# Kernel optimization log

Measured on AMD Instinct MI355X. Metric: run time of the kernel, lower is better.

Reference implementation:

```python
import jax, jax.numpy as jnp
import numpy as np
from functools import partial

VOCAB, D, H, L, T_MAX = 32000, 1024, 16, 8, 1024
HD = D // H
HIDDEN = int(D * 2.67)  # 2734, matches int(n_embd*hidden_mult)


def setup_inputs() -> dict:
    key = jax.random.key(0)
    ks = jax.random.split(key, 9)
    s = 0.02
    return {
        "idx": jax.random.randint(ks[0], (2, 1024), 0, VOCAB),
        "W_emb": jax.random.normal(ks[1], (VOCAB, D), jnp.float32) * s,  # tied with lm_head
        "norm1_w": jnp.ones((L, D), jnp.float32),
        "Wqkv": jax.random.normal(ks[2], (L, D, 3 * D), jnp.float32) * s,
        "Wout": jax.random.normal(ks[3], (L, D, D), jnp.float32) * s,
        "norm2_w": jnp.ones((L, D), jnp.float32),
        "Wg": jax.random.normal(ks[4], (L, D, HIDDEN), jnp.float32) * s,
        "Wu": jax.random.normal(ks[5], (L, D, HIDDEN), jnp.float32) * s,
        "Wd": jax.random.normal(ks[6], (L, HIDDEN, D), jnp.float32) * s,
        "final_norm_w": jnp.ones((D,), jnp.float32),
    }


def _rmsnorm(x, w, eps=1e-6):
    rms = jnp.sqrt(jnp.mean(x * x, axis=-1, keepdims=True) + eps)
    return x / rms * w


def _rope(x, cos_f, sin_f):
    # x: [B,H,T,hd]; cos_f/sin_f: [T, hd//2]
    x1, x2 = x[..., : HD // 2], x[..., HD // 2 :]
    c = cos_f[None, None]
    s = sin_f[None, None]
    return jnp.concatenate([x1 * c - x2 * s, x1 * s + x2 * c], axis=-1)


def _forward(idx, W_emb, norm1_w, Wqkv, Wout, norm2_w, Wg, Wu, Wd, final_norm_w):
    B, T = idx.shape
    # RoPE tables (buffers in the torch module)
    inv_freq = 1.0 / (10000.0 ** (jnp.arange(0, HD, 2, dtype=jnp.float32) / HD))
    ang = jnp.arange(T, dtype=jnp.float32)[:, None] * inv_freq[None, :]  # [T, hd//2]
    cos_f, sin_f = jnp.cos(ang), jnp.sin(ang)
    causal = jnp.tril(jnp.ones((T, T), dtype=bool))  # [T,T]
    scale = 1.0 / jnp.sqrt(jnp.float32(HD))

    def block(x, params):
        n1, wqkv, wout, n2, wg, wu, wd = params
        h = _rmsnorm(x, n1)
        qkv = (h @ wqkv).reshape(B, T, 3, H, HD).transpose(2, 0, 3, 1, 4)  # [3,B,H,T,hd]
        q, k, v = qkv[0], qkv[1], qkv[2]
        q = _rope(q, cos_f, sin_f)
        k = _rope(k, cos_f, sin_f)
        attn = jnp.einsum("bhqd,bhkd->bhqk", q, k) * scale
        attn = jnp.where(causal[None, None], attn, -jnp.inf)
        attn = jax.nn.softmax(attn, axis=-1)
        o = jnp.einsum("bhqk,bhkd->bhqd", attn, v)
        o = o.transpose(0, 2, 1, 3).reshape(B, T, D) @ wout
        x = x + o
        h2 = _rmsnorm(x, n2)
        x = x + (jax.nn.silu(h2 @ wg) * (h2 @ wu)) @ wd
        return x, None

    x = W_emb[idx]  # [B,T,D]
    x, _ = jax.lax.scan(block, x, (norm1_w, Wqkv, Wout, norm2_w, Wg, Wu, Wd))
    x = _rmsnorm(x, final_norm_w)
    return x @ W_emb.T  # tied lm_head -> [B,T,VOCAB]


def reference(idx, W_emb, norm1_w, Wqkv, Wout, norm2_w, Wg, Wu, Wd, final_norm_w):
    return _forward(idx, W_emb, norm1_w, Wqkv, Wout, norm2_w, Wg, Wu, Wd, final_norm_w)
```

## Files before the change

kernel.cpp:

```cpp
#include <hip/hip_runtime.h>
#include <cstdint>
#include <cmath>

#define D_MODEL 1024
#define T_SEQ   1024
#define NHEAD   16
#define NLAYER  8
#define HID     2734
#define HID_PAD 2816
#define NTOK    2048
#define VOCAB   32000

typedef __bf16 bf16x8 __attribute__((ext_vector_type(8)));
typedef __bf16 bf16x4 __attribute__((ext_vector_type(4)));
typedef float  f32x4  __attribute__((ext_vector_type(4)));

__device__ inline bf16x4 to_bf4(float a, float b, float c, float d) {
  bf16x4 t; t[0] = (__bf16)a; t[1] = (__bf16)b; t[2] = (__bf16)c; t[3] = (__bf16)d; return t;
}

__device__ inline void gload16(const __bf16* g, __bf16* l) {
  __builtin_amdgcn_global_load_lds(
      (const __attribute__((address_space(1))) void*)g,
      (__attribute__((address_space(3))) void*)l, 16, 0, 0);
}

__global__ __launch_bounds__(256) void embed_kernel(const int* __restrict__ idx,
                                                    const float* __restrict__ W,
                                                    float* __restrict__ x) {
  int t = blockIdx.x;
  int v = idx[t];
  float4 val = *(const float4*)&W[(size_t)v * D_MODEL + threadIdx.x * 4];
  *(float4*)&x[(size_t)t * D_MODEL + threadIdx.x * 4] = val;
}

__global__ __launch_bounds__(256) void rmsnorm_kernel(const float* __restrict__ x,
                                                      const float* __restrict__ w,
                                                      __bf16* __restrict__ out) {
  int row = blockIdx.x;
  int tid = threadIdx.x;
  float4 v = *(const float4*)&x[(size_t)row * D_MODEL + tid * 4];
  float s = v.x * v.x + v.y * v.y + v.z * v.z + v.w * v.w;
#pragma unroll
  for (int m = 32; m >= 1; m >>= 1) s += __shfl_xor(s, m, 64);
  __shared__ float red[4];
  if ((tid & 63) == 0) red[tid >> 6] = s;
  __syncthreads();
  float tot = red[0] + red[1] + red[2] + red[3];
  float inv = rsqrtf(tot * (1.0f / (float)D_MODEL) + 1e-6f);
  float4 wv = *(const float4*)&w[tid * 4];
  bf16x4 o4 = to_bf4(v.x * inv * wv.x, v.y * inv * wv.y, v.z * inv * wv.z, v.w * inv * wv.w);
  *(bf16x4*)&out[(size_t)row * D_MODEL + tid * 4] = o4;
}

__global__ __launch_bounds__(256) void rope_table_kernel(float* __restrict__ tab) {
  int p = blockIdx.x * 256 + threadIdx.x;
  int t = p >> 5, i = p & 31;
  float freq = exp2f(-(float)i * (13.287712379549449f / 32.0f));
  float sn, cs;
  sincosf((float)t * freq, &sn, &cs);
  tab[p] = cs;
  tab[32768 + p] = sn;
}

__global__ __launch_bounds__(256) void transpose_bf16_kernel(
    const float* __restrict__ in, __bf16* __restrict__ out,
    int R, int C, int Ro, int rmul, int roff) {
  __shared__ __bf16 tile[64][65];
  int r0 = blockIdx.x * 64, c0 = blockIdx.y * 64;
  int tid = threadIdx.x;
  bool fullc = (c0 + 64 <= C);
#pragma unroll
  for (int i = 0; i < 4; ++i) {
    int ri = i * 16 + (tid >> 4);
    int ci = (tid & 15) * 4;
    int r = r0 + ri;
    float4 v = {0.f, 0.f, 0.f, 0.f};
    if (r < R) {
      const float* p = in + (size_t)r * C + c0 + ci;
      if (fullc) {
        v = *(const float4*)p;
      } else {
        int c = c0 + ci;
        if (c + 0 < C) v.x = p[0];
        if (c + 1 < C) v.y = p[1];
        if (c + 2 < C) v.z = p[2];
        if (c + 3 < C) v.w = p[3];
      }
    }
    tile[ri][ci + 0] = (__bf16)v.x;
    tile[ri][ci + 1] = (__bf16)v.y;
    tile[ri][ci + 2] = (__bf16)v.z;
    tile[ri][ci + 3] = (__bf16)v.w;
  }
  __syncthreads();
#pragma unroll
  for (int i = 0; i < 4; ++i) {
    int oc = i * 16 + (tid >> 4);
    int orr = (tid & 15) * 4;
    bf16x4 t;
    t[0] = tile[orr + 0][oc];
    t[1] = tile[orr + 1][oc];
    t[2] = tile[orr + 2][oc];
    t[3] = tile[orr + 3][oc];
    *(bf16x4*)&out[((size_t)(c0 + oc) * rmul + roff) * Ro + r0 + orr] = t;
  }
}

__global__ __launch_bounds__(256) void convert_bf16_kernel(const float* __restrict__ in,
                                                           __bf16* __restrict__ out, int n4) {
  for (int i = blockIdx.x * 256 + threadIdx.x; i < n4; i += gridDim.x * 256) {
    float4 v = ((const float4*)in)[i];
    ((bf16x4*)out)[i] = to_bf4(v.x, v.y, v.z, v.w);
  }
}

template <int BM, int BN, int WM, int WN, int EPI>
__global__ __launch_bounds__(WM * WN * 64, 2) void gemm8(
    const __bf16* __restrict__ A, const __bf16* __restrict__ B,
    const float* __restrict__ Cin, void* __restrict__ Cout,
    int K, int ldc) {
  constexpr int NTH = WM * WN * 64;
  constexpr int MF = BM / (16 * WM);
  constexpr int MG = (MF + 3) / 4;
  constexpr int LA = (BM * 4) / NTH;
  constexpr int LB = (BN * 4) / NTH;
  static_assert(BN / WN == 64, "NF must be 4");
  __shared__ __align__(16) __bf16 lds[(BM + BN) * 128];

  const int tid = threadIdx.x;
  const int lane = tid & 63, wid = tid >> 6;
  const int wr = wid / WN, wn = wid % WN;
  const int lr = lane & 15, lg = lane >> 4;

  const int gx = gridDim.x;
  const int nwg = gx * gridDim.y;
  const int orig = blockIdx.y * gx + blockIdx.x;
  const int q = nwg >> 3, r8 = nwg & 7;
  const int xcd = orig & 7, loc = orig >> 3;
  const int swz = ((xcd < r8) ? xcd * (q + 1) : r8 * (q + 1) + (xcd - r8) * q) + loc;
  const int brow = (swz % gx) * BM;
  const int bcol = (swz / gx) * BN;

  const __bf16* pAg[LA];
  const __bf16* pBg[LB];
  int opA[LA], opB[LB];
#pragma unroll
  for (int i = 0; i < LA; ++i) {
    int p = tid + i * NTH;
    int row = ((p >> 6) << 4) | (p & 15), j = (p >> 4) & 3;
    pAg[i] = A + (size_t)(brow + row) * K + j * 8;
    opA[i] = p * 8;
  }
#pragma unroll
  for (int i = 0; i < LB; ++i) {
    int p = tid + i * NTH;
    int row = ((p >> 6) << 4) | (p & 15), j = (p >> 4) & 3;
    pBg[i] = B + (size_t)(bcol + row) * K + j * 8;
    opB[i] = p * 8;
  }

  const int ntiles = K >> 6;

  auto STAGE = [&](int v, int kkq) {
    int vs = v < ntiles ? v : ntiles - 1;
    int ko = vs * 64 + kkq * 32;
    int sa = (v & 1) * (BM * 64) + kkq * (BM * 32);
    int sb = BM * 128 + (v & 1) * (BN * 64) + kkq * (BN * 32);
#pragma unroll
    for (int i = 0; i < LA; ++i) gload16(pAg[i] + ko, lds + sa + opA[i]);
#pragma unroll
    for (int i = 0; i < LB; ++i) gload16(pBg[i] + ko, lds + sb + opB[i]);
  };

  f32x4 acc[MF][4];
#pragma unroll
  for (int m = 0; m < MF; ++m)
#pragma unroll
    for (int n = 0; n < 4; ++n) acc[m][n] = (f32x4){0.f, 0.f, 0.f, 0.f};

  STAGE(0, 0);
  STAGE(0, 1);
  STAGE(1, 0);

  const int fragoff = lg * 128 + lr * 8;

  for (int u = 0; u < ntiles; ++u) {
    const int buf = u & 1;
#pragma unroll
    for (int kk = 0; kk < 2; ++kk) {
      if constexpr (LA + LB == 3) asm volatile("s_waitcnt vmcnt(6)" ::: "memory");
      else                        asm volatile("s_waitcnt vmcnt(8)" ::: "memory");
      __builtin_amdgcn_sched_barrier(0);
      __builtin_amdgcn_s_barrier();
      __builtin_amdgcn_sched_barrier(0);
      if (kk == 0) STAGE(u + 1, 1);
      else         STAGE(u + 2, 0);
      const __bf16* Ab = lds + buf * (BM * 64) + kk * (BM * 32);
      const __bf16* Bb = lds + BM * 128 + buf * (BN * 64) + kk * (BN * 32);
      bf16x8 bfr[4];
#pragma unroll
      for (int n = 0; n < 4; ++n)
        bfr[n] = *(const bf16x8*)(Bb + (wn * 64 + n * 16) * 32 + fragoff);
#pragma unroll
      for (int mg = 0; mg < MG; ++mg) {
        bf16x8 afr[4];
#pragma unroll
        for (int i = 0; i < 4; ++i)
          afr[i] = *(const bf16x8*)(Ab + (wr * (BM / WM) + (mg * 4 + i) * 16) * 32 + fragoff);
        __builtin_amdgcn_s_setprio(1);
#pragma unroll
        for (int i = 0; i < 4; ++i)
#pragma unroll
          for (int n = 0; n < 4; ++n)
            acc[mg * 4 + i][n] =
                __builtin_amdgcn_mfma_f32_16x16x32_bf16(afr[i], bfr[n], acc[mg * 4 + i][n], 0, 0, 0);
        __builtin_amdgcn_s_setprio(0);
      }
    }
  }

#pragma unroll
  for (int m = 0; m < MF; ++m) {
#pragma unroll
    for (int n = 0; n < 4; ++n) {
#pragma unroll
      for (int rr = 0; rr < 4; ++rr) {
        int row = brow + wr * (BM / WM) + m * 16 + lg * 4 + rr;
        int col = bcol + wn * 64 + n * 16 + lr;
        size_t off = (size_t)row * ldc + col;
        float v = acc[m][n][rr];
        if (EPI == 0) {
          ((float*)Cout)[off] = v;
        } else if (EPI == 1) {
          ((float*)Cout)[off] = Cin[off] + v;
        } else if (EPI == 2) {
          float gv = Cin[off];
          ((__bf16*)Cout)[off] = (__bf16)(gv / (1.f + __expf(-gv)) * v);
        } else if (EPI == 3) {
          ((__bf16*)Cout)[off] = (__bf16)v;
        } else {
          float uv = __shfl_xor(v, 1);
          if ((lr & 1) == 0) {
            float r = v / (1.f + __expf(-v)) * uv;
            ((__bf16*)Cout)[(size_t)row * ldc + (col >> 1)] = (__bf16)r;
          }
        }
      }
    }
  }
}

__device__ inline void rope_chunk(const __bf16* p, const float* __restrict__ tab,
                                  int t, int d0, bf16x8& olo, bf16x8& ohi) {
  bf16x8 a8 = *(const bf16x8*)p;
  bf16x8 b8 = *(const bf16x8*)(p + 32);
  const float* ct = tab + t * 32 + d0;
  const float* st = tab + 32768 + t * 32 + d0;
  float4 c0 = *(const float4*)ct, c1 = *(const float4*)(ct + 4);
  float4 s0 = *(const float4*)st, s1 = *(const float4*)(st + 4);
  float cs[8] = {c0.x, c0.y, c0.z, c0.w, c1.x, c1.y, c1.z, c1.w};
  float ss[8] = {s0.x, s0.y, s0.z, s0.w, s1.x, s1.y, s1.z, s1.w};
#pragma unroll
  for (int j = 0; j < 8; ++j) {
    float av = (float)a8[j], bv = (float)b8[j];
    olo[j] = (__bf16)(av * cs[j] - bv * ss[j]);
    ohi[j] = (__bf16)(av * ss[j] + bv * cs[j]);
  }
}

__global__ __launch_bounds__(256) void prep_kernel(const __bf16* __restrict__ qkv,
                                                   const float* __restrict__ tab,
                                                   __bf16* __restrict__ Qr,
                                                   __bf16* __restrict__ Kr,
                                                   __bf16* __restrict__ Vt) {
  __shared__ __bf16 lsV[64][72];
  const int tid = threadIdx.x;
  const int bh = blockIdx.y, b = bh >> 4, h = bh & 15;
  const int t0 = blockIdx.x * 64;
  const size_t qbase = (size_t)b * T_SEQ * 3072 + h * 64;

  int row = tid >> 2, pc = tid & 3;
  int t = t0 + row;
  int tl = t & 1023;
  {
    int d0 = pc * 8;
    bf16x8 olo, ohi;
    rope_chunk(qkv + qbase + (size_t)t * 3072 + d0, tab, tl, d0, olo, ohi);
    __bf16* qo = Qr + ((size_t)bh * T_SEQ + t) * 64;
    *(bf16x8*)(qo + d0) = olo;
    *(bf16x8*)(qo + d0 + 32) = ohi;
    rope_chunk(qkv + qbase + (size_t)t * 3072 + 1024 + d0, tab, tl, d0, olo, ohi);
    __bf16* ko = Kr + ((size_t)bh * T_SEQ + t) * 64;
    *(bf16x8*)(ko + d0) = olo;
    *(bf16x8*)(ko + d0 + 32) = ohi;
  }
  {
    int c = pc * 16;
    bf16x8 v0 = *(const bf16x8*)(qkv + qbase + (size_t)t * 3072 + 2048 + c);
    bf16x8 v1 = *(const bf16x8*)(qkv + qbase + (size_t)t * 3072 + 2048 + c + 8);
    *(bf16x8*)&lsV[row][c] = v0;
    *(bf16x8*)&lsV[row][c + 8] = v1;
  }
  __syncthreads();
  {
    int d = tid >> 2, tc = (tid & 3) * 16;
    bf16x8 o0, o1;
#pragma unroll
    for (int j = 0; j < 8; ++j) o0[j] = lsV[tc + j][d];
#pragma unroll
    for (int j = 0; j < 8; ++j) o1[j] = lsV[tc + 8 + j][d];
    __bf16* vo = Vt + ((size_t)bh * 64 + d) * T_SEQ + t0 + tc;
    *(bf16x8*)vo = o0;
    *(bf16x8*)(vo + 8) = o1;
  }
}

__global__ __launch_bounds__(256) void attn_kernel(const __bf16* __restrict__ Qr,
                                                   const __bf16* __restrict__ Kr,
                                                   const __bf16* __restrict__ Vt,
                                                   __bf16* __restrict__ o) {
  __shared__ __align__(16) __bf16 lds[28672];
  const int tid = threadIdx.x;
  const int lane = tid & 63, w = tid >> 6;
  const int lr = lane & 15, lg = lane >> 4;
  const int bh = blockIdx.y, b = bh >> 4, h = bh & 15;
  const int qb = blockIdx.x, q0 = qb * 64;
  const __bf16* Qg = Qr + ((size_t)bh * T_SEQ + q0) * 64;
  const __bf16* Kg = Kr + (size_t)bh * T_SEQ * 64;
  const __bf16* Vg = Vt + (size_t)bh * 64 * T_SEQ;
  const float scale = 0.125f;

  {
    int row = ((tid >> 6) << 4) | (tid & 15);
    int j = (tid >> 4) & 3;
    gload16(Qg + row * 64 + j * 8, lds + tid * 8);
    gload16(Qg + row * 64 + 32 + j * 8, lds + 2048 + tid * 8);
  }

  f32x4 accO[4];
#pragma unroll
  for (int n = 0; n < 4; ++n) accO[n] = (f32x4){0.f, 0.f, 0.f, 0.f};
  float mrow[4], lrow[4];
#pragma unroll
  for (int r = 0; r < 4; ++r) { mrow[r] = -1e30f; lrow[r] = 0.f; }

  const int ntile = ((q0 + 63) >> 7) + 1;
  __bf16* Pw = lds + 20480 + w * 2048;

  for (int tt = 0; tt < ntile; ++tt) {
    const int j0 = tt * 128;
    __syncthreads();
#pragma unroll
    for (int i = 0; i < 2; ++i) {
      int p = tid + i * 256;
      int row = ((p >> 6) << 4) | (p & 15), j = (p >> 4) & 3;
      const __bf16* src = Kg + (size_t)(j0 + row) * 64 + j * 8;
      gload16(src, lds + 4096 + p * 8);
      gload16(src + 32, lds + 8192 + p * 8);
    }
#pragma unroll
    for (int s = 0; s < 4; ++s) {
      int d = ((tid >> 6) << 4) | (tid & 15), j = (tid >> 4) & 3;
      gload16(Vg + (size_t)d * T_SEQ + j0 + s * 32 + j * 8, lds + 12288 + s * 2048 + tid * 8);
    }
    __syncthreads();

    f32x4 s4[8];
#pragma unroll
    for (int n = 0; n < 8; ++n) s4[n] = (f32x4){0.f, 0.f, 0.f, 0.f};
#pragma unroll
    for (int kk = 0; kk < 2; ++kk) {
      bf16x8 aq = *(const bf16x8*)(lds + kk * 2048 + (w * 64 + lg * 16 + lr) * 8);
      __builtin_amdgcn_s_setprio(1);
#pragma unroll
      for (int jf = 0; jf < 8; ++jf) {
        bf16x8 bk = *(const bf16x8*)(lds + 4096 + kk * 4096 + (jf * 64 + lg * 16 + lr) * 8);
        s4[jf] = __builtin_amdgcn_mfma_f32_16x16x32_bf16(aq, bk, s4[jf], 0, 0, 0);
      }
      __builtin_amdgcn_s_setprio(0);
    }

    float pm[4];
#pragma unroll
    for (int r = 0; r < 4; ++r) pm[r] = -1e30f;
#pragma unroll
    for (int jf = 0; jf < 8; ++jf) {
      int gj = j0 + jf * 16 + lr;
#pragma unroll
      for (int r = 0; r < 4; ++r) {
        int gq = q0 + w * 16 + lg * 4 + r;
        float sv = s4[jf][r] * scale;
        if (gj > gq) sv = -1e30f;
        s4[jf][r] = sv;
        pm[r] = fmaxf(pm[r], sv);
      }
    }
#pragma unroll
    for (int r = 0; r < 4; ++r) {
#pragma unroll
      for (int m = 8; m >= 1; m >>= 1) pm[r] = fmaxf(pm[r], __shfl_xor(pm[r], m, 64));
    }
    float alpha[4];
#pragma unroll
    for (int r = 0; r < 4; ++r) {
      float mn = fmaxf(mrow[r], pm[r]);
      alpha[r] = expf(mrow[r] - mn);
      mrow[r] = mn;
    }
    float ps[4] = {0.f, 0.f, 0.f, 0.f};
#pragma unroll
    for (int jf = 0; jf < 8; ++jf) {
#pragma unroll
      for (int r = 0; r < 4; ++r) {
        float p = expf(s4[jf][r] - mrow[r]);
        s4[jf][r] = p;
        ps[r] += p;
      }
    }
#pragma unroll
    for (int r = 0; r < 4; ++r) {
#pragma unroll
      for (int m = 8; m >= 1; m >>= 1) ps[r] += __shfl_xor(ps[r], m, 64);
      lrow[r] = lrow[r] * alpha[r] + ps[r];
    }
#pragma unroll
    for (int n = 0; n < 4; ++n) {
#pragma unroll
      for (int r = 0; r < 4; ++r) accO[n][r] *= alpha[r];
    }

#pragma unroll
    for (int jf = 0; jf < 8; ++jf) {
      int s = jf >> 1;
      int rem = ((jf & 1) << 4) + lr;
      int base = s * 512 + (rem >> 3) * 128 + (rem & 7);
#pragma unroll
      for (int r = 0; r < 4; ++r) {
        int qloc = lg * 4 + r;
        Pw[base + qloc * 8] = (__bf16)s4[jf][r];
      }
    }
    asm volatile("s_waitcnt lgkmcnt(0)" ::: "memory");
    __builtin_amdgcn_sched_barrier(0);

#pragma unroll
    for (int s = 0; s < 4; ++s) {
      bf16x8 pa = *(const bf16x8*)(Pw + s * 512 + (lg * 16 + lr) * 8);
      __builtin_amdgcn_s_setprio(1);
#pragma unroll
      for (int nd = 0; nd < 4; ++nd) {
        bf16x8 bv = *(const bf16x8*)(lds + 12288 + s * 2048 + (nd * 64 + lg * 16 + lr) * 8);
        accO[nd] = __builtin_amdgcn_mfma_f32_16x16x32_bf16(pa, bv, accO[nd], 0, 0, 0);
      }
      __builtin_amdgcn_s_setprio(0);
    }
  }

#pragma unroll
  for (int nd = 0; nd < 4; ++nd) {
#pragma unroll
    for (int r = 0; r < 4; ++r) {
      int gq = q0 + w * 16 + lg * 4 + r;
      float val = accO[nd][r] / lrow[r];
      o[(size_t)(b * T_SEQ + gq) * D_MODEL + h * 64 + nd * 16 + lr] = (__bf16)val;
    }
  }
}

extern "C" void kernel_launch(void* const* d_in, const int* in_sizes, int n_in,
                              void* d_out, int out_size, void* d_ws, size_t ws_size,
                              hipStream_t stream) {
  const int*   idx     = (const int*)d_in[0];
  const float* W_emb   = (const float*)d_in[1];
  const float* norm1_w = (const float*)d_in[2];
  const float* Wqkv    = (const float*)d_in[3];
  const float* Wout    = (const float*)d_in[4];
  const float* norm2_w = (const float*)d_in[5];
  const float* Wg      = (const float*)d_in[6];
  const float* Wu      = (const float*)d_in[7];
  const float* Wd      = (const float*)d_in[8];
  const float* fnorm   = (const float*)d_in[9];
  float* out = (float*)d_out;

  float*  x    = (float*)d_ws;
  float*  tab  = x + (size_t)NTOK * D_MODEL;
  __bf16* qkvb = (__bf16*)(tab + 2 * 32768);
  __bf16* hb   = qkvb + (size_t)NTOK * 3 * D_MODEL;
  __bf16* ob   = hb + (size_t)NTOK * D_MODEL;
  __bf16* ga   = ob + (size_t)NTOK * D_MODEL;
  __bf16* Qrb  = ga + (size_t)NTOK * HID_PAD;
  __bf16* Krb  = Qrb + (size_t)32 * T_SEQ * 64;
  __bf16* Vtb  = Krb + (size_t)32 * T_SEQ * 64;
  __bf16* wbuf = Vtb + (size_t)32 * T_SEQ * 64;

  __bf16* wqkvT = wbuf;
  __bf16* woutT = wqkvT + (size_t)3 * D_MODEL * D_MODEL;
  __bf16* wguT  = woutT + (size_t)D_MODEL * D_MODEL;
  __bf16* wdT   = wguT + (size_t)2 * HID_PAD * D_MODEL;

  embed_kernel<<<NTOK, 256, 0, stream>>>(idx, W_emb, x);
  rope_table_kernel<<<128, 256, 0, stream>>>(tab);

  for (int l = 0; l < NLAYER; ++l) {
    transpose_bf16_kernel<<<dim3(16, 48), 256, 0, stream>>>(
        Wqkv + (size_t)l * D_MODEL * 3 * D_MODEL, wqkvT, D_MODEL, 3 * D_MODEL, D_MODEL, 1, 0);
    transpose_bf16_kernel<<<dim3(16, 16), 256, 0, stream>>>(
        Wout + (size_t)l * D_MODEL * D_MODEL, woutT, D_MODEL, D_MODEL, D_MODEL, 1, 0);
    transpose_bf16_kernel<<<dim3(16, 44), 256, 0, stream>>>(
        Wg + (size_t)l * D_MODEL * HID, wguT, D_MODEL, HID, D_MODEL, 2, 0);
    transpose_bf16_kernel<<<dim3(16, 44), 256, 0, stream>>>(
        Wu + (size_t)l * D_MODEL * HID, wguT, D_MODEL, HID, D_MODEL, 2, 1);
    transpose_bf16_kernel<<<dim3(44, 16), 256, 0, stream>>>(
        Wd + (size_t)l * HID * D_MODEL, wdT, HID, D_MODEL, HID_PAD, 1, 0);

    rmsnorm_kernel<<<NTOK, 256, 0, stream>>>(x, norm1_w + (size_t)l * D_MODEL, hb);
    gemm8<128, 256, 2, 4, 3><<<dim3(16, 12), 512, 0, stream>>>(
        hb, wqkvT, nullptr, qkvb, D_MODEL, 3 * D_MODEL);
    prep_kernel<<<dim3(16, 32), 256, 0, stream>>>(qkvb, tab, Qrb, Krb, Vtb);
    attn_kernel<<<dim3(16, 32), 256, 0, stream>>>(Qrb, Krb, Vtb, ob);
    gemm8<128, 128, 2, 2, 1><<<dim3(16, 8), 256, 0, stream>>>(
        ob, woutT, x, x, D_MODEL, D_MODEL);
    rmsnorm_kernel<<<NTOK, 256, 0, stream>>>(x, norm2_w + (size_t)l * D_MODEL, hb);
    gemm8<128, 256, 2, 4, 4><<<dim3(16, 22), 512, 0, stream>>>(
        hb, wguT, nullptr, ga, D_MODEL, HID_PAD);
    gemm8<128, 128, 2, 2, 1><<<dim3(16, 8), 256, 0, stream>>>(
        ga, wdT, x, x, HID_PAD, D_MODEL);
  }

  rmsnorm_kernel<<<NTOK, 256, 0, stream>>>(x, fnorm, hb);
  convert_bf16_kernel<<<2048, 256, 0, stream>>>(W_emb, wbuf, VOCAB * D_MODEL / 4);
  gemm8<256, 256, 2, 4, 0><<<dim3(8, 125), 512, 0, stream>>>(
      hb, wbuf, nullptr, out, D_MODEL, VOCAB);
}
```

Baseline: 2.104 ms.

## Fuse weight transposes, split A/B staging for 256-row GEMM, retile small GEMMs

The five per-layer weight transpose launches are merged into one kernel that selects its source matrix from the block index, cutting launch count. The GEMM staging is split into separate A and B loads. For 256-row tiles (MF==8) a new loop interleaves those loads with two half-MFMA phases separated by extra barriers and explicit lgkmcnt waits. The gate/up GEMM moves to 256x256 tiles, and the out-proj and down-proj GEMMs move to 128x64 tiles with twice as many blocks to fill more CUs. The extra barriers and larger tiles could add sync stalls or lower occupancy.

```diff
diff --git a/kernel.cpp b/kernel.cpp
--- a/kernel.cpp
+++ b/kernel.cpp
@@ -63,11 +63,23 @@
   tab[32768 + p] = sn;
 }
 
-__global__ __launch_bounds__(256) void transpose_bf16_kernel(
-    const float* __restrict__ in, __bf16* __restrict__ out,
-    int R, int C, int Ro, int rmul, int roff) {
+__global__ __launch_bounds__(256) void tp5_kernel(
+    const float* __restrict__ Wqkv, const float* __restrict__ Wout,
+    const float* __restrict__ Wg, const float* __restrict__ Wu,
+    const float* __restrict__ Wd,
+    __bf16* __restrict__ wqkvT, __bf16* __restrict__ woutT,
+    __bf16* __restrict__ wguT, __bf16* __restrict__ wdT) {
   __shared__ __bf16 tile[64][65];
-  int r0 = blockIdx.x * 64, c0 = blockIdx.y * 64;
+  int t = blockIdx.x;
+  const float* in;
+  __bf16* out;
+  int R, C, Ro, rmul, roff, tr;
+  if (t < 768)        { in = Wqkv; out = wqkvT; R = 1024; C = 3072; Ro = 1024; rmul = 1; roff = 0; tr = 16; }
+  else if (t < 1024)  { t -= 768;  in = Wout; out = woutT; R = 1024; C = 1024; Ro = 1024; rmul = 1; roff = 0; tr = 16; }
+  else if (t < 1728)  { t -= 1024; in = Wg; out = wguT; R = 1024; C = HID; Ro = 1024; rmul = 2; roff = 0; tr = 16; }
+  else if (t < 2432)  { t -= 1728; in = Wu; out = wguT; R = 1024; C = HID; Ro = 1024; rmul = 2; roff = 1; tr = 16; }
+  else                { t -= 2432; in = Wd; out = wdT; R = HID; C = 1024; Ro = HID_PAD; rmul = 1; roff = 0; tr = 44; }
+  int r0 = (t % tr) * 64, c0 = (t / tr) * 64;
   int tid = threadIdx.x;
   bool fullc = (c0 + 64 <= C);
 #pragma unroll
@@ -98,12 +110,12 @@
   for (int i = 0; i < 4; ++i) {
     int oc = i * 16 + (tid >> 4);
     int orr = (tid & 15) * 4;
-    bf16x4 t;
-    t[0] = tile[orr + 0][oc];
-    t[1] = tile[orr + 1][oc];
-    t[2] = tile[orr + 2][oc];
-    t[3] = tile[orr + 3][oc];
-    *(bf16x4*)&out[((size_t)(c0 + oc) * rmul + roff) * Ro + r0 + orr] = t;
+    bf16x4 tv;
+    tv[0] = tile[orr + 0][oc];
+    tv[1] = tile[orr + 1][oc];
+    tv[2] = tile[orr + 2][oc];
+    tv[3] = tile[orr + 3][oc];
+    *(bf16x4*)&out[((size_t)(c0 + oc) * rmul + roff) * Ro + r0 + orr] = tv;
   }
 }
 
@@ -123,6 +135,7 @@
   constexpr int NTH = WM * WN * 64;
   constexpr int MF = BM / (16 * WM);
   constexpr int MG = (MF + 3) / 4;
+  constexpr int CL = (MF < 4) ? MF : 4;
   constexpr int LA = (BM * 4) / NTH;
   constexpr int LB = (BN * 4) / NTH;
   static_assert(BN / WN == 64, "NF must be 4");
@@ -162,13 +175,17 @@
 
   const int ntiles = K >> 6;
 
-  auto STAGE = [&](int v, int kkq) {
+  auto STAGE_A = [&](int v, int kkq) {
     int vs = v < ntiles ? v : ntiles - 1;
     int ko = vs * 64 + kkq * 32;
     int sa = (v & 1) * (BM * 64) + kkq * (BM * 32);
+#pragma unroll
+    for (int i = 0; i < LA; ++i) gload16(pAg[i] + ko, lds + sa + opA[i]);
+  };
+  auto STAGE_B = [&](int v, int kkq) {
+    int vs = v < ntiles ? v : ntiles - 1;
+    int ko = vs * 64 + kkq * 32;
     int sb = BM * 128 + (v & 1) * (BN * 64) + kkq * (BN * 32);
-#pragma unroll
-    for (int i = 0; i < LA; ++i) gload16(pAg[i] + ko, lds + sa + opA[i]);
 #pragma unroll
     for (int i = 0; i < LB; ++i) gload16(pBg[i] + ko, lds + sb + opB[i]);
   };
@@ -179,43 +196,95 @@
 #pragma unroll
     for (int n = 0; n < 4; ++n) acc[m][n] = (f32x4){0.f, 0.f, 0.f, 0.f};
 
-  STAGE(0, 0);
-  STAGE(0, 1);
-  STAGE(1, 0);
+  STAGE_A(0, 0); STAGE_B(0, 0);
+  STAGE_A(0, 1); STAGE_B(0, 1);
+  STAGE_A(1, 0); STAGE_B(1, 0);
 
   const int fragoff = lg * 128 + lr * 8;
 
-  for (int u = 0; u < ntiles; ++u) {
-    const int buf = u & 1;
-#pragma unroll
-    for (int kk = 0; kk < 2; ++kk) {
-      if constexpr (LA + LB == 3) asm volatile("s_waitcnt vmcnt(6)" ::: "memory");
-      else                        asm volatile("s_waitcnt vmcnt(8)" ::: "memory");
-      __builtin_amdgcn_sched_barrier(0);
-      __builtin_amdgcn_s_barrier();
-      __builtin_amdgcn_sched_barrier(0);
-      if (kk == 0) STAGE(u + 1, 1);
-      else         STAGE(u + 2, 0);
-      const __bf16* Ab = lds + buf * (BM * 64) + kk * (BM * 32);
-      const __bf16* Bb = lds + BM * 128 + buf * (BN * 64) + kk * (BN * 32);
-      bf16x8 bfr[4];
-#pragma unroll
-      for (int n = 0; n < 4; ++n)
-        bfr[n] = *(const bf16x8*)(Bb + (wn * 64 + n * 16) * 32 + fragoff);
-#pragma unroll
-      for (int mg = 0; mg < MG; ++mg) {
-        bf16x8 afr[4];
+  if constexpr (MF == 8) {
+    for (int u = 0; u < ntiles; ++u) {
+      const int buf = u & 1;
+#pragma unroll
+      for (int kk = 0; kk < 2; ++kk) {
+        const int v = (kk == 0) ? u + 1 : u + 2;
+        const int kkq = kk ^ 1;
+        const __bf16* Ab = lds + buf * (BM * 64) + kk * (BM * 32);
+        const __bf16* Bb = lds + BM * 128 + buf * (BN * 64) + kk * (BN * 32);
+        asm volatile("s_waitcnt vmcnt(8)" ::: "memory");
+        __builtin_amdgcn_sched_barrier(0);
+        __builtin_amdgcn_s_barrier();
+        __builtin_amdgcn_sched_barrier(0);
+        STAGE_A(v, kkq);
+        bf16x8 bfr[4], af0[4];
+#pragma unroll
+        for (int n = 0; n < 4; ++n)
+          bfr[n] = *(const bf16x8*)(Bb + (wn * 64 + n * 16) * 32 + fragoff);
 #pragma unroll
         for (int i = 0; i < 4; ++i)
-          afr[i] = *(const bf16x8*)(Ab + (wr * (BM / WM) + (mg * 4 + i) * 16) * 32 + fragoff);
+          af0[i] = *(const bf16x8*)(Ab + (wr * 128 + i * 16) * 32 + fragoff);
+        asm volatile("s_waitcnt lgkmcnt(0)" ::: "memory");
+        __builtin_amdgcn_sched_barrier(0);
         __builtin_amdgcn_s_setprio(1);
 #pragma unroll
         for (int i = 0; i < 4; ++i)
 #pragma unroll
           for (int n = 0; n < 4; ++n)
-            acc[mg * 4 + i][n] =
-                __builtin_amdgcn_mfma_f32_16x16x32_bf16(afr[i], bfr[n], acc[mg * 4 + i][n], 0, 0, 0);
+            acc[i][n] = __builtin_amdgcn_mfma_f32_16x16x32_bf16(af0[i], bfr[n], acc[i][n], 0, 0, 0);
         __builtin_amdgcn_s_setprio(0);
+        __builtin_amdgcn_s_barrier();
+        STAGE_B(v, kkq);
+        bf16x8 af1[4];
+#pragma unroll
+        for (int i = 0; i < 4; ++i)
+          af1[i] = *(const bf16x8*)(Ab + (wr * 128 + 64 + i * 16) * 32 + fragoff);
+        asm volatile("s_waitcnt lgkmcnt(0)" ::: "memory");
+        __builtin_amdgcn_sched_barrier(0);
+        __builtin_amdgcn_s_setprio(1);
+#pragma unroll
+        for (int i = 0; i < 4; ++i)
+#pragma unroll
+          for (int n = 0; n < 4; ++n)
+            acc[4 + i][n] = __builtin_amdgcn_mfma_f32_16x16x32_bf16(af1[i], bfr[n], acc[4 + i][n], 0, 0, 0);
+        __builtin_amdgcn_s_setprio(0);
+        __builtin_amdgcn_s_barrier();
+      }
+    }
+  } else {
+    for (int u = 0; u < ntiles; ++u) {
+      const int buf = u & 1;
+#pragma unroll
+      for (int kk = 0; kk < 2; ++kk) {
+        if constexpr (LA + LB == 3) asm volatile("s_waitcnt vmcnt(6)" ::: "memory");
+        else                        asm volatile("s_waitcnt vmcnt(8)" ::: "memory");
+        __builtin_amdgcn_sched_barrier(0);
+        __builtin_amdgcn_s_barrier();
+        __builtin_amdgcn_sched_barrier(0);
+        const int v = (kk == 0) ? u + 1 : u + 2;
+        const int kkq = kk ^ 1;
+        STAGE_A(v, kkq);
+        STAGE_B(v, kkq);
+        const __bf16* Ab = lds + buf * (BM * 64) + kk * (BM * 32);
+        const __bf16* Bb = lds + BM * 128 + buf * (BN * 64) + kk * (BN * 32);
+        bf16x8 bfr[4];
+#pragma unroll
+        for (int n = 0; n < 4; ++n)
+          bfr[n] = *(const bf16x8*)(Bb + (wn * 64 + n * 16) * 32 + fragoff);
+#pragma unroll
+        for (int mg = 0; mg < MG; ++mg) {
+          bf16x8 afr[CL];
+#pragma unroll
+          for (int i = 0; i < CL; ++i)
+            afr[i] = *(const bf16x8*)(Ab + (wr * (BM / WM) + (mg * 4 + i) * 16) * 32 + fragoff);
+          __builtin_amdgcn_s_setprio(1);
+#pragma unroll
+          for (int i = 0; i < CL; ++i)
+#pragma unroll
+            for (int n = 0; n < 4; ++n)
+              acc[mg * 4 + i][n] =
+                  __builtin_amdgcn_mfma_f32_16x16x32_bf16(afr[i], bfr[n], acc[mg * 4 + i][n], 0, 0, 0);
+          __builtin_amdgcn_s_setprio(0);
+        }
       }
     }
   }
@@ -229,20 +298,20 @@
         int row = brow + wr * (BM / WM) + m * 16 + lg * 4 + rr;
         int col = bcol + wn * 64 + n * 16 + lr;
         size_t off = (size_t)row * ldc + col;
-        float v = acc[m][n][rr];
+        float vv = acc[m][n][rr];
         if (EPI == 0) {
-          ((float*)Cout)[off] = v;
+          ((float*)Cout)[off] = vv;
         } else if (EPI == 1) {
-          ((float*)Cout)[off] = Cin[off] + v;
+          ((float*)Cout)[off] = Cin[off] + vv;
         } else if (EPI == 2) {
           float gv = Cin[off];
-          ((__bf16*)Cout)[off] = (__bf16)(gv / (1.f + __expf(-gv)) * v);
+          ((__bf16*)Cout)[off] = (__bf16)(gv / (1.f + __expf(-gv)) * vv);
         } else if (EPI == 3) {
-          ((__bf16*)Cout)[off] = (__bf16)v;
+          ((__bf16*)Cout)[off] = (__bf16)vv;
         } else {
-          float uv = __shfl_xor(v, 1);
+          float uv = __shfl_xor(vv, 1);
           if ((lr & 1) == 0) {
-            float r = v / (1.f + __expf(-v)) * uv;
+            float r = vv / (1.f + __expf(-vv)) * uv;
             ((__bf16*)Cout)[(size_t)row * ldc + (col >> 1)] = (__bf16)r;
           }
         }
@@ -503,28 +572,25 @@
   rope_table_kernel<<<128, 256, 0, stream>>>(tab);
 
   for (int l = 0; l < NLAYER; ++l) {
-    transpose_bf16_kernel<<<dim3(16, 48), 256, 0, stream>>>(
-        Wqkv + (size_t)l * D_MODEL * 3 * D_MODEL, wqkvT, D_MODEL, 3 * D_MODEL, D_MODEL, 1, 0);
-    transpose_bf16_kernel<<<dim3(16, 16), 256, 0, stream>>>(
-        Wout + (size_t)l * D_MODEL * D_MODEL, woutT, D_MODEL, D_MODEL, D_MODEL, 1, 0);
-    transpose_bf16_kernel<<<dim3(16, 44), 256, 0, stream>>>(
-        Wg + (size_t)l * D_MODEL * HID, wguT, D_MODEL, HID, D_MODEL, 2, 0);
-    transpose_bf16_kernel<<<dim3(16, 44), 256, 0, stream>>>(
-        Wu + (size_t)l * D_MODEL * HID, wguT, D_MODEL, HID, D_MODEL, 2, 1);
-    transpose_bf16_kernel<<<dim3(44, 16), 256, 0, stream>>>(
-        Wd + (size_t)l * HID * D_MODEL, wdT, HID, D_MODEL, HID_PAD, 1, 0);
+    tp5_kernel<<<3136, 256, 0, stream>>>(
+        Wqkv + (size_t)l * D_MODEL * 3 * D_MODEL,
+        Wout + (size_t)l * D_MODEL * D_MODEL,
+        Wg + (size_t)l * D_MODEL * HID,
+        Wu + (size_t)l * D_MODEL * HID,
+        Wd + (size_t)l * HID * D_MODEL,
+        wqkvT, woutT, wguT, wdT);
 
     rmsnorm_kernel<<<NTOK, 256, 0, stream>>>(x, norm1_w + (size_t)l * D_MODEL, hb);
     gemm8<128, 256, 2, 4, 3><<<dim3(16, 12), 512, 0, stream>>>(
         hb, wqkvT, nullptr, qkvb, D_MODEL, 3 * D_MODEL);
     prep_kernel<<<dim3(16, 32), 256, 0, stream>>>(qkvb, tab, Qrb, Krb, Vtb);
     attn_kernel<<<dim3(16, 32), 256, 0, stream>>>(Qrb, Krb, Vtb, ob);
-    gemm8<128, 128, 2, 2, 1><<<dim3(16, 8), 256, 0, stream>>>(
+    gemm8<128, 64, 4, 1, 1><<<dim3(16, 16), 256, 0, stream>>>(
         ob, woutT, x, x, D_MODEL, D_MODEL);
     rmsnorm_kernel<<<NTOK, 256, 0, stream>>>(x, norm2_w + (size_t)l * D_MODEL, hb);
-    gemm8<128, 256, 2, 4, 4><<<dim3(16, 22), 512, 0, stream>>>(
+    gemm8<256, 256, 2, 4, 4><<<dim3(8, 22), 512, 0, stream>>>(
         hb, wguT, nullptr, ga, D_MODEL, HID_PAD);
-    gemm8<128, 128, 2, 2, 1><<<dim3(16, 8), 256, 0, stream>>>(
+    gemm8<128, 64, 4, 1, 1><<<dim3(16, 16), 256, 0, stream>>>(
         ga, wdT, x, x, HID_PAD, D_MODEL);
   }
 
```

New measurement: 1.780 ms. -15.4%, faster.
